# Optimization experiments

Hardware: AMD Instinct MI355X
Metric: run time of the kernel (lower is better)

The kernel has to match this reference:

```python
import jax, jax.numpy as jnp
import numpy as np

B, T, N, D, K, MP = 32, 50, 50000, 128, 16, 50
HID = (D + K) // 2  # WP_1 out features


def _normalize(x, axis=-1, eps=1e-12):
    return x / jnp.maximum(jnp.linalg.norm(x, axis=axis, keepdims=True), eps)


def _layer_norm(x, g, b, eps=1e-6):
    m = jnp.mean(x, axis=-1, keepdims=True)
    v = jnp.var(x, axis=-1, keepdims=True)
    return (x - m) * jax.lax.rsqrt(v + eps) * g + b


def setup_inputs() -> dict:
    key = jax.random.key(0)
    ks = jax.random.split(key, 20)
    std = 0.01
    session = jax.random.randint(ks[0], (B, T), 1, N + 1)  # ids >= 1, no padding
    lengths = jnp.full((B,), T, dtype=jnp.int32)
    isValidSession = jnp.ones((B * T,), dtype=bool)
    inp = {
        'session': session,
        'lengths': lengths,
        'tau': 1,
        'isValidSession': isValidSession,
        'train': 1,
        'I_emb': jax.random.normal(ks[1], (N + 1, D)) * std,
        'P_emb': jax.random.normal(ks[2], (K, D)) * std,
        'E_P_emb': jax.random.normal(ks[3], (MP, D)) * std,
        'E_S_emb': jax.random.normal(ks[4], (MP + 1, D)) * std,
        'V': _normalize(jax.random.normal(ks[5], (K, D))),
        'WP1': jax.random.normal(ks[6], (HID, D)),   # torch Linear weight [out, in]
        'WP2': jax.random.normal(ks[7], (K, HID)),
        'Wq': jax.random.normal(ks[8], (D, D)) / np.sqrt(D),
        'Wk': jax.random.normal(ks[9], (D, D)) / np.sqrt(D),
        'Wv': jax.random.normal(ks[10], (D, D)) / np.sqrt(D),
        'Wo': jax.random.normal(ks[11], (D, D)) / np.sqrt(D),
        'FF1': jax.random.normal(ks[12], (D, D)) / np.sqrt(D),
        'FF2': jax.random.normal(ks[13], (D, D)) / np.sqrt(D),
        'ln1_g': jnp.ones((D,)), 'ln1_b': jnp.zeros((D,)),
        'ln2_g': jnp.ones((D,)), 'ln2_b': jnp.zeros((D,)),
    }
    return inp


def _forward(session, lengths, tau, I_emb, P_emb, E_P_emb, E_S_emb, V,
             WP1, WP2, Wq, Wk, Wv, Wo, FF1, FF2, ln1_g, ln1_b, ln2_g, ln2_b):
    Vn = _normalize(V)                               # forward renormalizes V rows
    lf = lengths.astype(jnp.float32)
    isValidPos = (session != 0).astype(jnp.float32)  # [B,T]
    sess_emb = I_emb[session]                        # [B,T,D]
    EP = E_P_emb[jnp.arange(T) + (MP - T)]           # [T,D]
    es_idx = jnp.maximum(jnp.arange(T)[None, :] + 1 - (T - lengths[:, None]), 0)
    ES = E_S_emb[es_idx]                             # [B,T,D]

    # ---- ProxySelection (dropout in eval mode = identity) ----
    X = isValidPos[..., None] * (sess_emb + EP[None])
    X = jax.nn.leaky_relu(X @ WP1.T, 0.1) @ WP2.T    # [B,T,K]
    fP = jnp.sum(X, axis=1) / lf[:, None]
    pi = jax.nn.softmax(fP / tau, axis=-1)           # [B,K]
    p_s = pi @ P_emb                                 # [B,D]
    v = _normalize(pi @ Vn)                          # [B,D]

    # ---- SIE: single-layer self-attention encoder ----
    Xs = sess_emb + ES
    subseq = jnp.triu(jnp.ones((T, T), dtype=bool), 1)[None]        # causal
    pad = (session == 0)[:, None, :]                                # key padding
    mask = (subseq | pad)
    mask = mask.at[:, :, 0].set(False)
    non_pad = (session != 0).astype(jnp.float32)[..., None]
    q, kk, vv = Xs @ Wq.T, Xs @ Wk.T, Xs @ Wv.T
    scores = jnp.einsum('btd,bsd->bts', q, kk) / np.sqrt(D)
    scores = jnp.where(mask, -1e9, scores)
    attn = jax.nn.softmax(scores, axis=-1)
    h = (attn @ vv) @ Wo.T
    h = _layer_norm(h + Xs, ln1_g, ln1_b) * non_pad
    f = jax.nn.relu(h @ FF1.T) @ FF2.T
    s_s = _layer_norm(f + h, ln2_g, ln2_b) * non_pad                # [B,T,D]

    # project out v component per sample
    s_s_proj = s_s - v[:, None, :] * jnp.sum(v[:, None, :] * s_s, axis=-1, keepdims=True)
    orthogonal = jnp.abs(jnp.sum(v * p_s, axis=-1)) / jnp.linalg.norm(p_s, axis=-1)

    # ---- train_phase: dist(p_s+s_s_proj[b,t], I_proj_b) for all items ----
    # I_proj_b = I - v_b (v_b . I); with ||v_b||=1:
    #   ||F - I_proj||^2 = ||F||^2 - 2(F.I - (F.v)(v.I)) + ||I||^2 - (v.I)^2
    F = p_s[:, None, :] + s_s_proj                   # [B,T,D]
    vI = jnp.einsum('nd,bd->bn', I_emb, v)           # [B,N+1]
    Fv = jnp.einsum('btd,bd->bt', F, v)              # [B,T]
    FI = jnp.einsum('btd,nd->btn', F, I_emb)         # [B,T,N+1]
    Fn2 = jnp.sum(F * F, axis=-1)                    # [B,T]
    In2 = jnp.sum(I_emb * I_emb, axis=-1)[None, :] - vI * vI  # [B,N+1]
    dist = Fn2[..., None] - 2.0 * (FI - Fv[..., None] * vI[:, None, :]) + In2[:, None, :]
    return dist.reshape(B * T, N + 1), orthogonal


def reference(session, lengths, tau, isValidSession, train,
              I_emb, P_emb, E_P_emb, E_S_emb, V,
              WP1, WP2, Wq, Wk, Wv, Wo, FF1, FF2, ln1_g, ln1_b, ln2_g, ln2_b):
    # isValidSession is all-True and train=1: distance rows = all (b,t) pairs
    return _forward(session, lengths, tau, I_emb, P_emb, E_P_emb, E_S_emb, V,
                    WP1, WP2, Wq, Wk, Wv, Wo, FF1, FF2, ln1_g, ln1_b, ln2_g, ln2_b)
```

## Files before the change

kernel.cpp:

```cpp
#include <hip/hip_runtime.h>
#include <math.h>

#define B   32
#define T   50
#define N1  50001
#define D   128
#define KP  16
#define MP  50
#define HID 72
#define BT  (B*T)

typedef __attribute__((ext_vector_type(8))) short short8v;
typedef __attribute__((ext_vector_type(4))) float f32x4;

__device__ __forceinline__ unsigned short f2bf(float x) {
    unsigned u = __float_as_uint(x);
    u += 0x7fffu + ((u >> 16) & 1u);
    return (unsigned short)(u >> 16);
}

__device__ __forceinline__ float blockReduceSum128(float val, volatile float* sbuf) {
    for (int off = 32; off > 0; off >>= 1) val += __shfl_down(val, off, 64);
    __syncthreads();
    if ((threadIdx.x & 63) == 0) sbuf[threadIdx.x >> 6] = val;
    __syncthreads();
    return sbuf[0] + sbuf[1];
}

__global__ void k_fused_emb(const int* __restrict__ session,
                            const int* __restrict__ lengths,
                            const float* __restrict__ I_emb,
                            const float* __restrict__ EP_emb,
                            const float* __restrict__ ES_emb,
                            const float* __restrict__ WP1,
                            const float* __restrict__ WP2,
                            const float* __restrict__ Wq,
                            const float* __restrict__ Wk,
                            const float* __restrict__ Wv,
                            float* __restrict__ X2,
                            float* __restrict__ xs_o, float* __restrict__ q_o,
                            float* __restrict__ k_o, float* __restrict__ v_o) {
    int bt = blockIdx.x; int b = bt / T; int t = bt % T;
    int tid = threadIdx.x;
    __shared__ __align__(16) float x[D];
    __shared__ __align__(16) float xs[D];
    __shared__ float h[HID];
    int sid = session[bt];
    float ie = I_emb[(size_t)sid * D + tid];
    float xv_ = (sid != 0) ? (ie + EP_emb[(t + MP - T) * D + tid]) : 0.f;
    int es = t + 1 - (T - lengths[b]); if (es < 0) es = 0;
    float xsv = ie + ES_emb[es * D + tid];
    x[tid] = xv_;
    xs[tid] = xsv;
    __syncthreads();
    float aq = 0.f, ak = 0.f, av = 0.f;
    {
        const float4* wq4 = (const float4*)(Wq + tid * D);
        const float4* wk4 = (const float4*)(Wk + tid * D);
        const float4* wv4 = (const float4*)(Wv + tid * D);
        const float4* x4  = (const float4*)xs;
        #pragma unroll 8
        for (int k = 0; k < D / 4; ++k) {
            float4 xv = x4[k];
            float4 a = wq4[k], bq = wk4[k], c = wv4[k];
            aq += xv.x * a.x + xv.y * a.y + xv.z * a.z + xv.w * a.w;
            ak += xv.x * bq.x + xv.y * bq.y + xv.z * bq.z + xv.w * bq.w;
            av += xv.x * c.x + xv.y * c.y + xv.z * c.z + xv.w * c.w;
        }
    }
    if (tid < HID) {
        float acc = 0.f;
        const float4* w4 = (const float4*)(WP1 + tid * D);
        const float4* x4 = (const float4*)x;
        #pragma unroll 8
        for (int k = 0; k < D / 4; ++k) {
            float4 w = w4[k]; float4 xv = x4[k];
            acc += xv.x * w.x + xv.y * w.y + xv.z * w.z + xv.w * w.w;
        }
        h[tid] = acc > 0.f ? acc : 0.1f * acc;
    }
    xs_o[bt * D + tid] = xsv;
    q_o[bt * D + tid] = aq; k_o[bt * D + tid] = ak; v_o[bt * D + tid] = av;
    __syncthreads();
    if (tid < KP) {
        float acc = 0.f;
        const float* w = WP2 + tid * HID;
        for (int k = 0; k < HID; ++k) acc += h[k] * w[k];
        X2[bt * KP + tid] = acc;
    }
}

__global__ void k_proxy_head(const float* __restrict__ X2,
                             const int* __restrict__ lengths,
                             const int* __restrict__ tau_i,
                             const float* __restrict__ P_emb,
                             const float* __restrict__ V,
                             float* __restrict__ ps_o,
                             float* __restrict__ v_o,
                             float* __restrict__ orth_o) {
    int b = blockIdx.x; int tid = threadIdx.x;
    __shared__ float pi[KP];
    __shared__ float vn[KP];
    __shared__ float sbuf[2];
    float tau = (float)tau_i[0];
    float lf = (float)lengths[b];
    if (tid < KP) {
        float s = 0.f;
        for (int t = 0; t < T; ++t) s += X2[(b * T + t) * KP + tid];
        pi[tid] = (s / lf) / tau;
    }
    if (tid < KP) {
        float s = 0.f;
        for (int d = 0; d < D; ++d) { float z = V[tid * D + d]; s += z * z; }
        vn[tid] = fmaxf(sqrtf(s), 1e-12f);
    }
    __syncthreads();
    if (tid == 0) {
        float m = pi[0];
        for (int k = 1; k < KP; ++k) m = fmaxf(m, pi[k]);
        float s = 0.f;
        for (int k = 0; k < KP; ++k) { float e = expf(pi[k] - m); pi[k] = e; s += e; }
        for (int k = 0; k < KP; ++k) pi[k] /= s;
    }
    __syncthreads();
    float p = 0.f, vt = 0.f;
    for (int k = 0; k < KP; ++k) {
        p  += pi[k] * P_emb[k * D + tid];
        vt += pi[k] * (V[k * D + tid] / vn[k]);
    }
    float vsq = blockReduceSum128(vt * vt, sbuf);
    float vv = vt / fmaxf(sqrtf(vsq), 1e-12f);
    float psq = blockReduceSum128(p * p, sbuf);
    float dvp = blockReduceSum128(vv * p, sbuf);
    ps_o[b * D + tid] = p;
    v_o[b * D + tid] = vv;
    if (tid == 0) orth_o[b] = fabsf(dvp) / sqrtf(psq);
}

__global__ void k_fused_attn(const int* __restrict__ session,
                             const float* __restrict__ q,
                             const float* __restrict__ kk,
                             const float* __restrict__ vv,
                             const float* __restrict__ xs,
                             const float* __restrict__ Wo,
                             const float* __restrict__ g1, const float* __restrict__ b1,
                             const float* __restrict__ FF1, const float* __restrict__ FF2,
                             const float* __restrict__ g2, const float* __restrict__ b2,
                             const float* __restrict__ ps, const float* __restrict__ v,
                             short* __restrict__ G16, float* __restrict__ Fn2) {
    int bt = blockIdx.x; int b = bt / T; int t = bt % T;
    int tid = threadIdx.x;
    __shared__ __align__(16) float qs[D];
    __shared__ __align__(16) float buf1[D];
    __shared__ __align__(16) float buf2[D];
    __shared__ float attn[64];
    __shared__ float sbuf[2];
    qs[tid] = q[bt * D + tid];
    __syncthreads();
    if (tid < T) {
        int s = tid;
        bool allowed = (s == 0) || ((s <= t) && (session[b * T + s] != 0));
        float sc = -1e9f;
        if (allowed) {
            float a = 0.f;
            const float4* kr = (const float4*)(kk + (size_t)(b * T + s) * D);
            const float4* q4 = (const float4*)qs;
            #pragma unroll 8
            for (int d = 0; d < D / 4; ++d) {
                float4 kv = kr[d]; float4 qv = q4[d];
                a += qv.x * kv.x + qv.y * kv.y + qv.z * kv.z + qv.w * kv.w;
            }
            sc = a * 0.088388347648318447f;
        }
        attn[s] = sc;
    }
    __syncthreads();
    if (tid < 64) {
        float vsc = (tid < T) ? attn[tid] : -1e30f;
        float m = vsc;
        for (int off = 32; off > 0; off >>= 1) m = fmaxf(m, __shfl_xor(m, off, 64));
        float e = (tid < T) ? expf(vsc - m) : 0.f;
        float ssum = e;
        for (int off = 32; off > 0; off >>= 1) ssum += __shfl_xor(ssum, off, 64);
        if (tid < T) attn[tid] = e / ssum;
    }
    __syncthreads();
    float acc = 0.f;
    for (int s = 0; s < T; ++s) acc += attn[s] * vv[(size_t)(b * T + s) * D + tid];
    buf1[tid] = acc;
    __syncthreads();
    float a = 0.f;
    {
        const float4* w4 = (const float4*)(Wo + tid * D);
        const float4* h4 = (const float4*)buf1;
        #pragma unroll 8
        for (int k = 0; k < D / 4; ++k) {
            float4 w = w4[k]; float4 hv = h4[k];
            a += hv.x * w.x + hv.y * w.y + hv.z * w.z + hv.w * w.w;
        }
    }
    float x1 = a + xs[bt * D + tid];
    float mean = blockReduceSum128(x1, sbuf) * (1.f / D);
    float dx = x1 - mean;
    float var = blockReduceSum128(dx * dx, sbuf) * (1.f / D);
    float hx = (dx * rsqrtf(var + 1e-6f) * g1[tid] + b1[tid]) * ((session[bt] != 0) ? 1.f : 0.f);
    buf2[tid] = hx;
    __syncthreads();
    float a1 = 0.f;
    {
        const float4* w4 = (const float4*)(FF1 + tid * D);
        const float4* h4 = (const float4*)buf2;
        #pragma unroll 8
        for (int k = 0; k < D / 4; ++k) {
            float4 w = w4[k]; float4 hv = h4[k];
            a1 += hv.x * w.x + hv.y * w.y + hv.z * w.z + hv.w * w.w;
        }
    }
    __syncthreads();
    buf1[tid] = fmaxf(a1, 0.f);
    __syncthreads();
    float f = 0.f;
    {
        const float4* w4 = (const float4*)(FF2 + tid * D);
        const float4* t4 = (const float4*)buf1;
        #pragma unroll 8
        for (int k = 0; k < D / 4; ++k) {
            float4 w = w4[k]; float4 tv = t4[k];
            f += tv.x * w.x + tv.y * w.y + tv.z * w.z + tv.w * w.w;
        }
    }
    float x2 = f + hx;
    float mean2 = blockReduceSum128(x2, sbuf) * (1.f / D);
    float dx2 = x2 - mean2;
    float var2 = blockReduceSum128(dx2 * dx2, sbuf) * (1.f / D);
    float ss = dx2 * rsqrtf(var2 + 1e-6f) * g2[tid] + b2[tid];
    ss *= (session[bt] != 0) ? 1.f : 0.f;
    float vb = v[b * D + tid];
    float vs = blockReduceSum128(vb * ss, sbuf);
    float ssp = ss - vb * vs;
    float Fd = ps[b * D + tid] + ssp;
    float Fv = blockReduceSum128(Fd * vb, sbuf);
    float Gd = Fd - Fv * vb;
    float fn2 = blockReduceSum128(Fd * Fd, sbuf);
    G16[bt * D + tid] = (short)f2bf(Gd);
    if (tid == 0) Fn2[bt] = fn2;
}

#define LDK 136

__global__ __launch_bounds__(256) void k_item_mfma(const float* __restrict__ I,
                                                   const float* __restrict__ v,
                                                   float* __restrict__ In2pb,
                                                   unsigned short* __restrict__ I16) {
    __shared__ __align__(16) short Is[64][LDK];
    __shared__ __align__(16) short Vs[32][LDK];
    __shared__ float sq[64][4];
    __shared__ float in2[64];
    int n0 = blockIdx.x * 64;
    int tid = threadIdx.x;
    {
        int vr = tid >> 3;
        int vc = (tid & 7) * 16;
        const float4* src = (const float4*)&v[vr * D + vc];
        #pragma unroll
        for (int s = 0; s < 4; ++s) {
            float4 f = src[s];
            ushort4 u;
            u.x = f2bf(f.x); u.y = f2bf(f.y); u.z = f2bf(f.z); u.w = f2bf(f.w);
            *(ushort4*)&Vs[vr][vc + s * 4] = u;
        }
    }
    {
        int r = tid >> 2;
        int qq = tid & 3;
        int n = n0 + r;
        float ss = 0.f;
        if (n < N1) {
            const float4* src = (const float4*)&I[(size_t)n * D + qq * 32];
            #pragma unroll
            for (int s = 0; s < 8; ++s) {
                float4 f = src[s];
                ss += f.x * f.x + f.y * f.y + f.z * f.z + f.w * f.w;
                ushort4 u;
                u.x = f2bf(f.x); u.y = f2bf(f.y); u.z = f2bf(f.z); u.w = f2bf(f.w);
                *(ushort4*)&Is[r][qq * 32 + s * 4] = u;
                *(ushort4*)&I16[(size_t)n * D + qq * 32 + s * 4] = u;
            }
        } else {
            #pragma unroll
            for (int s = 0; s < 8; ++s)
                *(ushort4*)&Is[r][qq * 32 + s * 4] = make_ushort4(0, 0, 0, 0);
        }
        sq[r][qq] = ss;
    }
    __syncthreads();
    if (tid < 64) in2[tid] = sq[tid][0] + sq[tid][1] + sq[tid][2] + sq[tid][3];
    __syncthreads();
    int w = tid >> 6, l = tid & 63, lr = l & 15, lg = l >> 4;
    f32x4 acc[2] = {{0.f,0.f,0.f,0.f},{0.f,0.f,0.f,0.f}};
    short8v af[4];
    #pragma unroll
    for (int ks = 0; ks < 4; ++ks)
        af[ks] = *(const short8v*)&Is[w * 16 + lr][ks * 32 + lg * 8];
    #pragma unroll
    for (int nt = 0; nt < 2; ++nt) {
        #pragma unroll
        for (int ks = 0; ks < 4; ++ks) {
            short8v bf = *(const short8v*)&Vs[nt * 16 + lr][ks * 32 + lg * 8];
            acc[nt] = __builtin_amdgcn_mfma_f32_16x16x32_bf16(af[ks], bf, acc[nt], 0, 0, 0);
        }
    }
    #pragma unroll
    for (int nt = 0; nt < 2; ++nt) {
        int b = nt * 16 + lr;
        #pragma unroll
        for (int i = 0; i < 4; ++i) {
            int item = w * 16 + lg * 4 + i;
            int n = n0 + item;
            if (n < N1) {
                float dvi = acc[nt][i];
                In2pb[(size_t)b * N1 + n] = in2[item] - dvi * dvi;
            }
        }
    }
}

__global__ __launch_bounds__(256) void k_dist_mfma(const short* __restrict__ G16,
                                                   const unsigned short* __restrict__ I16,
                                                   const float* __restrict__ Fn2,
                                                   const float* __restrict__ In2pb,
                                                   float* __restrict__ out) {
    __shared__ __align__(16) short As[128][LDK];
    __shared__ __align__(16) short Bs[64][LDK];
    int n0  = blockIdx.x * 64;
    int bt0 = blockIdx.y * 128;
    int tid = threadIdx.x;
    int r = tid >> 4;
    int c = (tid & 15) * 8;
    #pragma unroll
    for (int s = 0; s < 8; ++s) {
        int row = r + s * 16;
        short8v gv = {};
        if (bt0 + row < BT) gv = *(const short8v*)&G16[(size_t)(bt0 + row) * D + c];
        *(short8v*)&As[row][c] = gv;
    }
    #pragma unroll
    for (int s = 0; s < 4; ++s) {
        int row = r + s * 16;
        int n = n0 + row;
        short8v bv = {};
        if (n < N1) bv = *(const short8v*)&I16[(size_t)n * D + c];
        *(short8v*)&Bs[row][c] = bv;
    }
    __syncthreads();
    int w  = tid >> 6;
    int l  = tid & 63;
    int lr = l & 15;
    int lg = l >> 4;
    short8v af[2][4];
    #pragma unroll
    for (int mi = 0; mi < 2; ++mi)
        #pragma unroll
        for (int ks = 0; ks < 4; ++ks)
            af[mi][ks] = *(const short8v*)&As[w * 32 + mi * 16 + lr][ks * 32 + lg * 8];
    f32x4 acc[2][4];
    #pragma unroll
    for (int mi = 0; mi < 2; ++mi)
        #pragma unroll
        for (int nt = 0; nt < 4; ++nt) acc[mi][nt] = (f32x4){0.f, 0.f, 0.f, 0.f};
    #pragma unroll
    for (int nt = 0; nt < 4; ++nt) {
        short8v bf[4];
        #pragma unroll
        for (int ks = 0; ks < 4; ++ks)
            bf[ks] = *(const short8v*)&Bs[nt * 16 + lr][ks * 32 + lg * 8];
        #pragma unroll
        for (int mi = 0; mi < 2; ++mi)
            #pragma unroll
            for (int ks = 0; ks < 4; ++ks)
                acc[mi][nt] = __builtin_amdgcn_mfma_f32_16x16x32_bf16(af[mi][ks], bf[ks], acc[mi][nt], 0, 0, 0);
    }
    #pragma unroll
    for (int mi = 0; mi < 2; ++mi) {
        int rb = bt0 + w * 32 + mi * 16 + lg * 4;
        if (rb < BT) {
            float4 fn4 = *(const float4*)&Fn2[rb];
            float fnv[4] = {fn4.x, fn4.y, fn4.z, fn4.w};
            #pragma unroll
            for (int i = 0; i < 4; ++i) {
                int row = rb + i;
                int b = row / T;
                const float* inrow = In2pb + (size_t)b * N1;
                float* orow = out + (size_t)row * N1;
                #pragma unroll
                for (int nt = 0; nt < 4; ++nt) {
                    int col = n0 + nt * 16 + lr;
                    if (col < N1) orow[col] = fnv[i] + inrow[col] - 2.f * acc[mi][nt][i];
                }
            }
        }
    }
}

extern "C" void kernel_launch(void* const* d_in, const int* in_sizes, int n_in,
                              void* d_out, int out_size, void* d_ws, size_t ws_size,
                              hipStream_t stream) {
    const int*   session = (const int*)d_in[0];
    const int*   lengths = (const int*)d_in[1];
    const int*   tau     = (const int*)d_in[2];
    const float* I_emb   = (const float*)d_in[5];
    const float* P_emb   = (const float*)d_in[6];
    const float* EP      = (const float*)d_in[7];
    const float* ES      = (const float*)d_in[8];
    const float* V       = (const float*)d_in[9];
    const float* WP1     = (const float*)d_in[10];
    const float* WP2     = (const float*)d_in[11];
    const float* Wq      = (const float*)d_in[12];
    const float* Wk      = (const float*)d_in[13];
    const float* Wv      = (const float*)d_in[14];
    const float* Wo      = (const float*)d_in[15];
    const float* FF1     = (const float*)d_in[16];
    const float* FF2     = (const float*)d_in[17];
    const float* g1      = (const float*)d_in[18];
    const float* b1      = (const float*)d_in[19];
    const float* g2      = (const float*)d_in[20];
    const float* b2      = (const float*)d_in[21];
    float* out = (float*)d_out;
    float* ws  = (float*)d_ws;

    float* wsX2   = ws;
    float* wsPs   = wsX2 + 25600;
    float* wsV    = wsPs + 4096;
    float* wsXs   = wsV + 4096;
    float* wsQ    = wsXs + 204800;
    float* wsK    = wsQ + 204800;
    float* wsVv   = wsK + 204800;
    float* wsFn2  = wsVv + 204800;
    float* wsIn2  = wsFn2 + 1600;
    short* wsG16  = (short*)(wsIn2 + 1600032);
    unsigned short* wsI16 = (unsigned short*)(wsG16 + 204800);

    float* orth_out = out + (size_t)BT * N1;

    k_fused_emb <<<BT, 128, 0, stream>>>(session, lengths, I_emb, EP, ES,
                                         WP1, WP2, Wq, Wk, Wv,
                                         wsX2, wsXs, wsQ, wsK, wsVv);
    k_proxy_head<<<B, 128, 0, stream>>>(wsX2, lengths, tau, P_emb, V, wsPs, wsV, orth_out);
    k_fused_attn<<<BT, 128, 0, stream>>>(session, wsQ, wsK, wsVv, wsXs,
                                         Wo, g1, b1, FF1, FF2, g2, b2,
                                         wsPs, wsV, wsG16, wsFn2);
    k_item_mfma <<<(N1 + 63) / 64, 256, 0, stream>>>(I_emb, wsV, wsIn2, wsI16);
    dim3 gdist((N1 + 63) / 64, (BT + 127) / 128);
    k_dist_mfma <<<gdist, 256, 0, stream>>>(wsG16, wsI16, wsFn2, wsIn2, out);
}
```

Measured before the change: 308.5 us.

## Stream A fragments from global and stage In2 rows in LDS for dist kernel

```diff
diff --git a/kernel.cpp b/kernel.cpp
--- a/kernel.cpp
+++ b/kernel.cpp
@@ -325,77 +325,71 @@
     }
 }
 
-__global__ __launch_bounds__(256) void k_dist_mfma(const short* __restrict__ G16,
-                                                   const unsigned short* __restrict__ I16,
-                                                   const float* __restrict__ Fn2,
-                                                   const float* __restrict__ In2pb,
-                                                   float* __restrict__ out) {
-    __shared__ __align__(16) short As[128][LDK];
+__global__ __launch_bounds__(256, 6) void k_dist_mfma(const short* __restrict__ G16,
+                                                      const unsigned short* __restrict__ I16,
+                                                      const float* __restrict__ Fn2,
+                                                      const float* __restrict__ In2pb,
+                                                      float* __restrict__ out) {
     __shared__ __align__(16) short Bs[64][LDK];
+    __shared__ float in2s[4][64];
     int n0  = blockIdx.x * 64;
     int bt0 = blockIdx.y * 128;
     int tid = threadIdx.x;
-    int r = tid >> 4;
-    int c = (tid & 15) * 8;
-    #pragma unroll
-    for (int s = 0; s < 8; ++s) {
-        int row = r + s * 16;
-        short8v gv = {};
-        if (bt0 + row < BT) gv = *(const short8v*)&G16[(size_t)(bt0 + row) * D + c];
-        *(short8v*)&As[row][c] = gv;
-    }
-    #pragma unroll
-    for (int s = 0; s < 4; ++s) {
-        int row = r + s * 16;
-        int n = n0 + row;
-        short8v bv = {};
-        if (n < N1) bv = *(const short8v*)&I16[(size_t)n * D + c];
-        *(short8v*)&Bs[row][c] = bv;
+    int b_lo = bt0 / T;
+    {
+        int r = tid >> 4;
+        int c = (tid & 15) * 8;
+        #pragma unroll
+        for (int s = 0; s < 4; ++s) {
+            int row = r + s * 16;
+            int n = n0 + row;
+            short8v bv = {};
+            if (n < N1) bv = *(const short8v*)&I16[(size_t)n * D + c];
+            *(short8v*)&Bs[row][c] = bv;
+        }
+    }
+    {
+        int bb = tid >> 6, cl = tid & 63;
+        int b = b_lo + bb; if (b > B - 1) b = B - 1;
+        int col = n0 + cl;
+        in2s[bb][cl] = (col < N1) ? In2pb[(size_t)b * N1 + col] : 0.f;
     }
     __syncthreads();
     int w  = tid >> 6;
     int l  = tid & 63;
     int lr = l & 15;
     int lg = l >> 4;
-    short8v af[2][4];
-    #pragma unroll
-    for (int mi = 0; mi < 2; ++mi)
-        #pragma unroll
-        for (int ks = 0; ks < 4; ++ks)
-            af[mi][ks] = *(const short8v*)&As[w * 32 + mi * 16 + lr][ks * 32 + lg * 8];
-    f32x4 acc[2][4];
-    #pragma unroll
-    for (int mi = 0; mi < 2; ++mi)
-        #pragma unroll
-        for (int nt = 0; nt < 4; ++nt) acc[mi][nt] = (f32x4){0.f, 0.f, 0.f, 0.f};
-    #pragma unroll
-    for (int nt = 0; nt < 4; ++nt) {
-        short8v bf[4];
-        #pragma unroll
-        for (int ks = 0; ks < 4; ++ks)
-            bf[ks] = *(const short8v*)&Bs[nt * 16 + lr][ks * 32 + lg * 8];
-        #pragma unroll
-        for (int mi = 0; mi < 2; ++mi)
-            #pragma unroll
-            for (int ks = 0; ks < 4; ++ks)
-                acc[mi][nt] = __builtin_amdgcn_mfma_f32_16x16x32_bf16(af[mi][ks], bf[ks], acc[mi][nt], 0, 0, 0);
-    }
     #pragma unroll
     for (int mi = 0; mi < 2; ++mi) {
-        int rb = bt0 + w * 32 + mi * 16 + lg * 4;
+        int rbase = bt0 + w * 32 + mi * 16;
+        short8v af[4];
+        const short* arow = &G16[(size_t)(rbase + lr) * D];
+        #pragma unroll
+        for (int ks = 0; ks < 4; ++ks)
+            af[ks] = *(const short8v*)&arow[ks * 32 + lg * 8];
+        f32x4 acc[4] = {{0.f,0.f,0.f,0.f},{0.f,0.f,0.f,0.f},{0.f,0.f,0.f,0.f},{0.f,0.f,0.f,0.f}};
+        #pragma unroll
+        for (int nt = 0; nt < 4; ++nt) {
+            #pragma unroll
+            for (int ks = 0; ks < 4; ++ks) {
+                short8v bf = *(const short8v*)&Bs[nt * 16 + lr][ks * 32 + lg * 8];
+                acc[nt] = __builtin_amdgcn_mfma_f32_16x16x32_bf16(af[ks], bf, acc[nt], 0, 0, 0);
+            }
+        }
+        int rb = rbase + lg * 4;
         if (rb < BT) {
             float4 fn4 = *(const float4*)&Fn2[rb];
             float fnv[4] = {fn4.x, fn4.y, fn4.z, fn4.w};
             #pragma unroll
             for (int i = 0; i < 4; ++i) {
                 int row = rb + i;
-                int b = row / T;
-                const float* inrow = In2pb + (size_t)b * N1;
+                int bb = row / T - b_lo;
                 float* orow = out + (size_t)row * N1;
                 #pragma unroll
                 for (int nt = 0; nt < 4; ++nt) {
-                    int col = n0 + nt * 16 + lr;
-                    if (col < N1) orow[col] = fnv[i] + inrow[col] - 2.f * acc[mi][nt][i];
+                    int cl = nt * 16 + lr;
+                    int col = n0 + cl;
+                    if (col < N1) orow[col] = fnv[i] + in2s[bb][cl] - 2.f * acc[nt][i];
                 }
             }
         }
@@ -438,7 +432,7 @@
     float* wsFn2  = wsVv + 204800;
     float* wsIn2  = wsFn2 + 1600;
     short* wsG16  = (short*)(wsIn2 + 1600032);
-    unsigned short* wsI16 = (unsigned short*)(wsG16 + 204800);
+    unsigned short* wsI16 = (unsigned short*)(wsG16 + 212992);
 
     float* orth_out = out + (size_t)BT * N1;
 
```

New measurement: 342.4 us. 1.11x slower.
